# Optimization experiments

Measured on AMD Instinct MI355X. Metric: run time of the kernel, lower is better.

Reference implementation:

```python
import jax, jax.numpy as jnp
import numpy as np

N = 10000      # num nodes
E = 160000     # num edges (before self-loops)
D_IN = 512
D_HID = 512
D_OUT = 512
C = 64         # num classes


def setup_inputs() -> dict:
    key = jax.random.key(0)
    ks = jax.random.split(key, 8)
    x = jax.random.normal(ks[0], (N, D_IN), dtype=jnp.float32)
    edge_index = jax.random.randint(ks[1], (2, E), 0, N, dtype=jnp.int64)
    W1 = jax.random.normal(ks[2], (D_IN, D_HID), jnp.float32) / np.sqrt(D_IN)
    b1 = jnp.zeros((D_HID,), jnp.float32)
    W2 = jax.random.normal(ks[3], (D_HID, D_OUT), jnp.float32) / np.sqrt(D_HID)
    b2 = jnp.zeros((D_OUT,), jnp.float32)
    Wc = jax.random.normal(ks[4], (D_OUT, C), jnp.float32) / np.sqrt(D_OUT)
    bc = jnp.zeros((C,), jnp.float32)
    return {"x": x, "edge_index": edge_index, "W1": W1, "b1": b1,
            "W2": W2, "b2": b2, "Wc": Wc, "bc": bc}


def _gcn_conv(x, src, dst, ew, W, b):
    """GCNConv: symmetric degree-normalized scatter-add. ew = edge weights."""
    h = x @ W  # [N, D_out] dense GEMM
    deg = jax.ops.segment_sum(ew, dst, num_segments=N)  # in-degree incl. loops
    dis = jnp.where(deg > 0, jax.lax.rsqrt(jnp.maximum(deg, 1e-12)), 0.0)
    norm = dis[src] * dis[dst] * ew  # [E+N]
    out = jax.ops.segment_sum(h[src] * norm[:, None], dst, num_segments=N)
    return out + b


def reference(x, edge_index, W1, b1, W2, b2, Wc, bc):
    src, dst = edge_index[0], edge_index[1]
    # add_remaining_self_loops: drop existing self-loops, add one per node
    loops = jnp.arange(N, dtype=edge_index.dtype)
    src_f = jnp.concatenate([src, loops])
    dst_f = jnp.concatenate([dst, loops])
    ew = jnp.concatenate([(src != dst).astype(jnp.float32),
                          jnp.ones((N,), jnp.float32)])
    h = jax.nn.relu(_gcn_conv(x, src_f, dst_f, ew, W1, b1))
    h = _gcn_conv(h, src_f, dst_f, ew, W2, b2)
    logits = h @ Wc + bc
    return logits, jax.nn.log_softmax(logits, axis=1)
```

## Files before the change

### kernel.cpp

```cpp
#include <hip/hip_runtime.h>
#include <hip/hip_bf16.h>

#define N_NODES 10000
#define DIM 512
#define NCLS 64
#define BM 64
#define BN 128
#define BK 32
#define ELLW 64

typedef __hip_bfloat16 bf16;
typedef unsigned short u16;
typedef __attribute__((ext_vector_type(8))) short short8;
typedef __attribute__((ext_vector_type(4))) float f32x4;

__device__ __forceinline__ float b2f(bf16 v) { return __bfloat162float(v); }
__device__ __forceinline__ float ldIn(const void* p, size_t i, int isb) {
    return isb ? b2f(((const bf16*)p)[i]) : ((const float*)p)[i];
}
__device__ __forceinline__ int getE(const int* ei, int is64, int flat) {
    return is64 ? ei[2 * (size_t)flat] : ei[flat];
}
__device__ __forceinline__ void load_lds16(const bf16* g, bf16* l) {
    __builtin_amdgcn_global_load_lds(
        (const __attribute__((address_space(1))) void*)g,
        (__attribute__((address_space(3))) void*)l, 16, 0, 0);
}

__global__ void init_kernel(const u16* x16, const int* ei, int* flags, int* cursor) {
    int i = blockIdx.x * blockDim.x + threadIdx.x;
    if (i < N_NODES) cursor[i] = 0;
    if (blockIdx.x == 0 && threadIdx.x < 64) {
        int l = threadIdx.x;
        int cf = 0;
        #pragma unroll
        for (int j = 0; j < 4; j++) {
            int e = (x16[l * 4 + j] >> 7) & 0xFF;
            cf += (e >= 97 && e <= 157) ? 1 : 0;
        }
        #pragma unroll
        for (int o = 32; o > 0; o >>= 1) cf += __shfl_xor(cf, o, 64);
        int cz = (l < 32) ? ((ei[2 * l + 1] == 0) ? 1 : 0) : 0;
        #pragma unroll
        for (int o = 32; o > 0; o >>= 1) cz += __shfl_xor(cz, o, 64);
        if (l == 0) { flags[0] = (cf >= 200) ? 1 : 0; flags[1] = (cz >= 16) ? 1 : 0; }
    }
}

__global__ void fill_ell(const int* __restrict__ ei, const int* __restrict__ flags,
                         int* __restrict__ cursor, int* __restrict__ ell, int E) {
    int e = blockIdx.x * blockDim.x + threadIdx.x;
    if (e >= E) return;
    int is64 = flags[1];
    int s = getE(ei, is64, e), d = getE(ei, is64, E + e);
    if (s == d || (unsigned)s >= N_NODES || (unsigned)d >= N_NODES) return;
    int pos = atomicAdd(&cursor[d], 1);
    ell[d * ELLW + (pos & (ELLW - 1))] = s;
}

__global__ __launch_bounds__(256) void convert_all(
        const void* __restrict__ X, const void* __restrict__ W1,
        const void* __restrict__ W2, const void* __restrict__ Wc,
        const int* __restrict__ flags, const int* __restrict__ cursor,
        bf16* __restrict__ Xb, bf16* __restrict__ Wt1, bf16* __restrict__ Wt2,
        bf16* __restrict__ Wtc, float* __restrict__ dis) {
    __shared__ float tile[32][33];
    int b = blockIdx.x, t = threadIdx.x;
    int isb = flags[0];
    if (b < 2500) {
        int base = (b * 256 + t) * 8;
        bf16 o[8];
        if (isb) {
            *(uint4*)o = *(const uint4*)((const bf16*)X + base);
        } else {
            const float* Xf = (const float*)X + base;
            float4 v0 = *(const float4*)Xf, v1 = *(const float4*)(Xf + 4);
            o[0] = __float2bfloat16(v0.x); o[1] = __float2bfloat16(v0.y);
            o[2] = __float2bfloat16(v0.z); o[3] = __float2bfloat16(v0.w);
            o[4] = __float2bfloat16(v1.x); o[5] = __float2bfloat16(v1.y);
            o[6] = __float2bfloat16(v1.z); o[7] = __float2bfloat16(v1.w);
        }
        *(uint4*)&Xb[base] = *(uint4*)o;
    } else if (b < 3044) {
        const void* W; bf16* Wt; int N; int bb;
        if (b < 2756)      { W = W1; Wt = Wt1; N = DIM;  bb = b - 2500; }
        else if (b < 3012) { W = W2; Wt = Wt2; N = DIM;  bb = b - 2756; }
        else               { W = Wc; Wt = Wtc; N = NCLS; bb = b - 3012; }
        int nt = N / 32;
        int n0 = (bb % nt) * 32, k0 = (bb / nt) * 32;
        int tx = t & 31, ty = t >> 5;
        for (int r = ty; r < 32; r += 8)
            tile[r][tx] = ldIn(W, (size_t)(k0 + r) * N + n0 + tx, isb);
        __syncthreads();
        for (int r = ty; r < 32; r += 8)
            Wt[(size_t)(n0 + r) * DIM + k0 + tx] = __float2bfloat16(tile[tx][r]);
    } else {
        int base = ((b - 3044) * 256 + t) * 8;
        #pragma unroll
        for (int j = 0; j < 8; j++) {
            int n = base + j;
            if (n < N_NODES) dis[n] = rsqrtf((float)cursor[n] + 1.0f);
        }
    }
}

__global__ __launch_bounds__(256) void gemm_mfma(
        const bf16* __restrict__ A, const bf16* __restrict__ Bt,
        bf16* __restrict__ C, int M, int Nc, int K,
        const float* __restrict__ rowscale) {
    __shared__ bf16 At[BM * BK];
    __shared__ bf16 Bts[BN * BK];
    int t = threadIdx.x;
    int w = t >> 6, l = t & 63;
    int bm = blockIdx.y * BM, bn = blockIdx.x * BN;
    int wn = w * 32;

    f32x4 acc[4][2] = {};
    int srow = l >> 2;
    int sk8  = (l & 3) * 8;

    for (int k0 = 0; k0 < K; k0 += BK) {
        __syncthreads();
        load_lds16(A + (size_t)(bm + w * 16 + srow) * K + k0 + sk8, &At[w * 512]);
        #pragma unroll
        for (int half = 0; half < 2; half++) {
            int c = w + half * 4;
            load_lds16(Bt + (size_t)(bn + c * 16 + srow) * K + k0 + sk8, &Bts[c * 512]);
        }
        __syncthreads();

        short8 af[4], bf[2];
        #pragma unroll
        for (int i = 0; i < 4; i++)
            af[i] = *(const short8*)&At[(i * 16 + (l & 15)) * BK + (l >> 4) * 8];
        #pragma unroll
        for (int j = 0; j < 2; j++)
            bf[j] = *(const short8*)&Bts[(wn + j * 16 + (l & 15)) * BK + (l >> 4) * 8];
        #pragma unroll
        for (int i = 0; i < 4; i++)
            #pragma unroll
            for (int j = 0; j < 2; j++)
                acc[i][j] = __builtin_amdgcn_mfma_f32_16x16x32_bf16(
                                af[i], bf[j], acc[i][j], 0, 0, 0);
    }

    int col = l & 15, rq = (l >> 4) * 4;
    #pragma unroll
    for (int i = 0; i < 4; i++) {
        #pragma unroll
        for (int r = 0; r < 4; r++) {
            int gm = bm + i * 16 + rq + r;
            if (gm >= M) continue;
            float rs = rowscale ? rowscale[gm] : 1.0f;
            #pragma unroll
            for (int j = 0; j < 2; j++) {
                int gn = bn + wn + j * 16 + col;
                C[(size_t)gm * Nc + gn] = __float2bfloat16(acc[i][j][r] * rs);
            }
        }
    }
}

__global__ __launch_bounds__(256) void gather_ell(
        const int* __restrict__ cursor, const int* __restrict__ ell,
        const bf16* __restrict__ Hs, const float* __restrict__ dis,
        const void* __restrict__ bias, const int* __restrict__ flags,
        bf16* __restrict__ Out, int relu) {
    int wid = (int)((blockIdx.x * (size_t)blockDim.x + threadIdx.x) >> 6);
    int lane = threadIdx.x & 63;
    if (wid >= N_NODES) return;
    int cnt = min(cursor[wid], ELLW);
    int idx = ell[wid * ELLW + lane];

    float acc[8];
    bf16 v[8];
    *(uint4*)v = *(const uint4*)(Hs + (size_t)wid * DIM + lane * 8);
    #pragma unroll
    for (int j = 0; j < 8; j++) acc[j] = b2f(v[j]);

    int e = 0;
    for (; e + 7 < cnt; e += 8) {
        bf16 r[8][8];
        #pragma unroll
        for (int b = 0; b < 8; b++) {
            int s = __shfl(idx, e + b, 64);
            *(uint4*)r[b] = *(const uint4*)(Hs + (size_t)s * DIM + lane * 8);
        }
        #pragma unroll
        for (int j = 0; j < 8; j++)
            acc[j] += ((b2f(r[0][j]) + b2f(r[1][j])) + (b2f(r[2][j]) + b2f(r[3][j])))
                    + ((b2f(r[4][j]) + b2f(r[5][j])) + (b2f(r[6][j]) + b2f(r[7][j])));
    }
    for (; e < cnt; e++) {
        int s = __shfl(idx, e, 64);
        *(uint4*)v = *(const uint4*)(Hs + (size_t)s * DIM + lane * 8);
        #pragma unroll
        for (int j = 0; j < 8; j++) acc[j] += b2f(v[j]);
    }

    float ds = dis[wid];
    int ibias = flags[0];
    bf16 o[8];
    #pragma unroll
    for (int j = 0; j < 8; j++) {
        float val = acc[j] * ds + ldIn(bias, lane * 8 + j, ibias);
        if (relu) val = fmaxf(val, 0.0f);
        o[j] = __float2bfloat16(val);
    }
    *(uint4*)(Out + (size_t)wid * DIM + lane * 8) = *(uint4*)o;
}

__global__ __launch_bounds__(256) void cls_lsm_kernel(
        const bf16* __restrict__ A, const bf16* __restrict__ Wct,
        const void* __restrict__ bias, const int* __restrict__ flags,
        float* __restrict__ out, int M) {
    __shared__ bf16 Ws[NCLS * DIM];
    int t = threadIdx.x, w = t >> 6, l = t & 63;

    #pragma unroll
    for (int i = 0; i < 16; i++) {
        int c = i * 4 + w;
        load_lds16(Wct + c * 512 + l * 8, &Ws[c * 512]);
    }
    __syncthreads();

    int row0 = (blockIdx.x * 4 + w) * 16;
    int q = l >> 4, col15 = l & 15;

    f32x4 acc[4] = {};
    #pragma unroll
    for (int k0 = 0; k0 < DIM; k0 += 32) {
        short8 af = *(const short8*)&A[(size_t)(row0 + col15) * DIM + k0 + q * 8];
        #pragma unroll
        for (int j = 0; j < 4; j++) {
            short8 bf = *(const short8*)&Ws[(j * 16 + col15) * DIM + k0 + q * 8];
            acc[j] = __builtin_amdgcn_mfma_f32_16x16x32_bf16(af, bf, acc[j], 0, 0, 0);
        }
    }

    int ibias = flags[0];
    float bcol[4];
    #pragma unroll
    for (int j = 0; j < 4; j++) bcol[j] = ldIn(bias, j * 16 + col15, ibias);

    #pragma unroll
    for (int r = 0; r < 4; r++) {
        int row = row0 + q * 4 + r;
        float v[4];
        #pragma unroll
        for (int j = 0; j < 4; j++) v[j] = acc[j][r] + bcol[j];
        float m = fmaxf(fmaxf(v[0], v[1]), fmaxf(v[2], v[3]));
        #pragma unroll
        for (int o = 8; o > 0; o >>= 1) m = fmaxf(m, __shfl_xor(m, o, 64));
        float s = __expf(v[0] - m) + __expf(v[1] - m) + __expf(v[2] - m) + __expf(v[3] - m);
        #pragma unroll
        for (int o = 8; o > 0; o >>= 1) s += __shfl_xor(s, o, 64);
        float lse = m + __logf(s);
        if (row < M) {
            #pragma unroll
            for (int j = 0; j < 4; j++) {
                out[(size_t)row * NCLS + j * 16 + col15] = v[j];
                out[(size_t)M * NCLS + (size_t)row * NCLS + j * 16 + col15] = v[j] - lse;
            }
        }
    }
}

extern "C" void kernel_launch(void* const* d_in, const int* in_sizes, int n_in,
                              void* d_out, int out_size, void* d_ws, size_t ws_size,
                              hipStream_t stream) {
    const void* x  = d_in[0];
    const int*  ei = (const int*)d_in[1];
    const void* W1 = d_in[2];
    const void* b1 = d_in[3];
    const void* W2 = d_in[4];
    const void* b2 = d_in[5];
    const void* Wc = d_in[6];
    const void* bc = d_in[7];
    float* out = (float*)d_out;
    int E = in_sizes[1] / 2;

    char* ws = (char*)d_ws;
    int*   flags  = (int*)ws;
    float* dis    = (float*)(ws + 4096);
    int*   cursor = (int*)(ws + 65536);
    int*   ell    = (int*)(ws + 131072);
    bf16*  xb     = (bf16*) (ws + 4194304);
    bf16*  Wt1    = (bf16*) (ws + 14680064);
    bf16*  Wt2    = (bf16*) (ws + 15204352);
    bf16*  Wct    = (bf16*) (ws + 15728640);
    bf16*  B0     = (bf16*) (ws + 16777216);
    bf16*  B1     = (bf16*) (ws + 27262976);

    int gE = (E + 255) / 256;
    int gN = (N_NODES * 64 + 255) / 256;
    dim3 gg(DIM / BN, (N_NODES + BM - 1) / BM);

    init_kernel<<<(N_NODES + 255) / 256, 256, 0, stream>>>((const u16*)x, ei, flags, cursor);
    fill_ell<<<gE, 256, 0, stream>>>(ei, flags, cursor, ell, E);
    convert_all<<<3049, 256, 0, stream>>>(x, W1, W2, Wc, flags, cursor,
                                          xb, Wt1, Wt2, Wct, dis);

    gemm_mfma<<<gg, 256, 0, stream>>>(xb, Wt1, B0, N_NODES, DIM, DIM, dis);
    gather_ell<<<gN, 256, 0, stream>>>(cursor, ell, B0, dis, b1, flags, B1, 1);

    gemm_mfma<<<gg, 256, 0, stream>>>(B1, Wt2, B0, N_NODES, DIM, DIM, dis);
    gather_ell<<<gN, 256, 0, stream>>>(cursor, ell, B0, dis, b2, flags, B1, 0);

    cls_lsm_kernel<<<(N_NODES + 63) / 64, 256, 0, stream>>>(B1, Wct, bc, flags, out, N_NODES);
}
```

Baseline: 192.2 us.

## Fuse ELL fill into convert kernel, recompute degree scale inline, widen GEMM K tile

Moves the ELL-building edge scatter into the convert_all launch as extra blocks, which removes one kernel launch. The dis array is dropped and the normalization factor is recomputed from cursor in the GEMM epilogue and in the gather. The GEMM K tile grows from 32 to 64, halving the K-loop iterations and barriers at the cost of more LDS per block. The classifier kernel becomes one wave per 16 rows reading Wc directly from global memory instead of staging it in LDS.

```diff
diff --git a/kernel.cpp b/kernel.cpp
--- a/kernel.cpp
+++ b/kernel.cpp
@@ -6,7 +6,7 @@
 #define NCLS 64
 #define BM 64
 #define BN 128
-#define BK 32
+#define BK 64
 #define ELLW 64
 
 typedef __hip_bfloat16 bf16;
@@ -47,27 +47,17 @@
     }
 }
 
-__global__ void fill_ell(const int* __restrict__ ei, const int* __restrict__ flags,
-                         int* __restrict__ cursor, int* __restrict__ ell, int E) {
-    int e = blockIdx.x * blockDim.x + threadIdx.x;
-    if (e >= E) return;
-    int is64 = flags[1];
-    int s = getE(ei, is64, e), d = getE(ei, is64, E + e);
-    if (s == d || (unsigned)s >= N_NODES || (unsigned)d >= N_NODES) return;
-    int pos = atomicAdd(&cursor[d], 1);
-    ell[d * ELLW + (pos & (ELLW - 1))] = s;
-}
-
 __global__ __launch_bounds__(256) void convert_all(
         const void* __restrict__ X, const void* __restrict__ W1,
         const void* __restrict__ W2, const void* __restrict__ Wc,
-        const int* __restrict__ flags, const int* __restrict__ cursor,
+        const int* __restrict__ ei, const int* __restrict__ flags,
+        int* __restrict__ cursor, int* __restrict__ ell,
         bf16* __restrict__ Xb, bf16* __restrict__ Wt1, bf16* __restrict__ Wt2,
-        bf16* __restrict__ Wtc, float* __restrict__ dis) {
+        bf16* __restrict__ Wtc, int E) {
     __shared__ float tile[32][33];
     int b = blockIdx.x, t = threadIdx.x;
-    int isb = flags[0];
     if (b < 2500) {
+        int isb = flags[0];
         int base = (b * 256 + t) * 8;
         bf16 o[8];
         if (isb) {
@@ -82,6 +72,7 @@
         }
         *(uint4*)&Xb[base] = *(uint4*)o;
     } else if (b < 3044) {
+        int isb = flags[0];
         const void* W; bf16* Wt; int N; int bb;
         if (b < 2756)      { W = W1; Wt = Wt1; N = DIM;  bb = b - 2500; }
         else if (b < 3012) { W = W2; Wt = Wt2; N = DIM;  bb = b - 2756; }
@@ -95,19 +86,20 @@
         for (int r = ty; r < 32; r += 8)
             Wt[(size_t)(n0 + r) * DIM + k0 + tx] = __float2bfloat16(tile[tx][r]);
     } else {
-        int base = ((b - 3044) * 256 + t) * 8;
-        #pragma unroll
-        for (int j = 0; j < 8; j++) {
-            int n = base + j;
-            if (n < N_NODES) dis[n] = rsqrtf((float)cursor[n] + 1.0f);
-        }
+        int e = (b - 3044) * 256 + t;
+        if (e >= E) return;
+        int is64 = flags[1];
+        int s = getE(ei, is64, e), d = getE(ei, is64, E + e);
+        if (s == d || (unsigned)s >= N_NODES || (unsigned)d >= N_NODES) return;
+        int pos = atomicAdd(&cursor[d], 1);
+        ell[d * ELLW + (pos & (ELLW - 1))] = s;
     }
 }
 
 __global__ __launch_bounds__(256) void gemm_mfma(
         const bf16* __restrict__ A, const bf16* __restrict__ Bt,
         bf16* __restrict__ C, int M, int Nc, int K,
-        const float* __restrict__ rowscale) {
+        const int* __restrict__ deg) {
     __shared__ bf16 At[BM * BK];
     __shared__ bf16 Bts[BN * BK];
     int t = threadIdx.x;
@@ -116,32 +108,39 @@
     int wn = w * 32;
 
     f32x4 acc[4][2] = {};
-    int srow = l >> 2;
-    int sk8  = (l & 3) * 8;
+    int srow8 = l >> 3;
+    int sk8b  = (l & 7) * 8;
 
     for (int k0 = 0; k0 < K; k0 += BK) {
         __syncthreads();
-        load_lds16(A + (size_t)(bm + w * 16 + srow) * K + k0 + sk8, &At[w * 512]);
-        #pragma unroll
-        for (int half = 0; half < 2; half++) {
-            int c = w + half * 4;
-            load_lds16(Bt + (size_t)(bn + c * 16 + srow) * K + k0 + sk8, &Bts[c * 512]);
+        #pragma unroll
+        for (int i = 0; i < 2; i++) {
+            int c = w * 2 + i;
+            load_lds16(A + (size_t)(bm + c * 8 + srow8) * K + k0 + sk8b, &At[c * 512]);
+        }
+        #pragma unroll
+        for (int i = 0; i < 4; i++) {
+            int c = w * 4 + i;
+            load_lds16(Bt + (size_t)(bn + c * 8 + srow8) * K + k0 + sk8b, &Bts[c * 512]);
         }
         __syncthreads();
 
-        short8 af[4], bf[2];
-        #pragma unroll
-        for (int i = 0; i < 4; i++)
-            af[i] = *(const short8*)&At[(i * 16 + (l & 15)) * BK + (l >> 4) * 8];
-        #pragma unroll
-        for (int j = 0; j < 2; j++)
-            bf[j] = *(const short8*)&Bts[(wn + j * 16 + (l & 15)) * BK + (l >> 4) * 8];
-        #pragma unroll
-        for (int i = 0; i < 4; i++)
+        #pragma unroll
+        for (int kk = 0; kk < BK; kk += 32) {
+            short8 af[4], bf[2];
+            #pragma unroll
+            for (int i = 0; i < 4; i++)
+                af[i] = *(const short8*)&At[(i * 16 + (l & 15)) * BK + kk + (l >> 4) * 8];
             #pragma unroll
             for (int j = 0; j < 2; j++)
-                acc[i][j] = __builtin_amdgcn_mfma_f32_16x16x32_bf16(
-                                af[i], bf[j], acc[i][j], 0, 0, 0);
+                bf[j] = *(const short8*)&Bts[(wn + j * 16 + (l & 15)) * BK + kk + (l >> 4) * 8];
+            #pragma unroll
+            for (int i = 0; i < 4; i++)
+                #pragma unroll
+                for (int j = 0; j < 2; j++)
+                    acc[i][j] = __builtin_amdgcn_mfma_f32_16x16x32_bf16(
+                                    af[i], bf[j], acc[i][j], 0, 0, 0);
+        }
     }
 
     int col = l & 15, rq = (l >> 4) * 4;
@@ -151,7 +150,7 @@
         for (int r = 0; r < 4; r++) {
             int gm = bm + i * 16 + rq + r;
             if (gm >= M) continue;
-            float rs = rowscale ? rowscale[gm] : 1.0f;
+            float rs = rsqrtf((float)deg[gm] + 1.0f);
             #pragma unroll
             for (int j = 0; j < 2; j++) {
                 int gn = bn + wn + j * 16 + col;
@@ -163,13 +162,13 @@
 
 __global__ __launch_bounds__(256) void gather_ell(
         const int* __restrict__ cursor, const int* __restrict__ ell,
-        const bf16* __restrict__ Hs, const float* __restrict__ dis,
-        const void* __restrict__ bias, const int* __restrict__ flags,
-        bf16* __restrict__ Out, int relu) {
+        const bf16* __restrict__ Hs, const void* __restrict__ bias,
+        const int* __restrict__ flags, bf16* __restrict__ Out, int relu) {
     int wid = (int)((blockIdx.x * (size_t)blockDim.x + threadIdx.x) >> 6);
     int lane = threadIdx.x & 63;
     if (wid >= N_NODES) return;
-    int cnt = min(cursor[wid], ELLW);
+    int cnt0 = cursor[wid];
+    int cnt = min(cnt0, ELLW);
     int idx = ell[wid * ELLW + lane];
 
     float acc[8];
@@ -198,7 +197,7 @@
         for (int j = 0; j < 8; j++) acc[j] += b2f(v[j]);
     }
 
-    float ds = dis[wid];
+    float ds = rsqrtf((float)cnt0 + 1.0f);
     int ibias = flags[0];
     bf16 o[8];
     #pragma unroll
@@ -210,30 +209,21 @@
     *(uint4*)(Out + (size_t)wid * DIM + lane * 8) = *(uint4*)o;
 }
 
-__global__ __launch_bounds__(256) void cls_lsm_kernel(
+__global__ __launch_bounds__(64) void cls_lsm_kernel(
         const bf16* __restrict__ A, const bf16* __restrict__ Wct,
         const void* __restrict__ bias, const int* __restrict__ flags,
         float* __restrict__ out, int M) {
-    __shared__ bf16 Ws[NCLS * DIM];
-    int t = threadIdx.x, w = t >> 6, l = t & 63;
-
-    #pragma unroll
-    for (int i = 0; i < 16; i++) {
-        int c = i * 4 + w;
-        load_lds16(Wct + c * 512 + l * 8, &Ws[c * 512]);
-    }
-    __syncthreads();
-
-    int row0 = (blockIdx.x * 4 + w) * 16;
+    int l = threadIdx.x;
+    int row0 = blockIdx.x * 16;
     int q = l >> 4, col15 = l & 15;
 
     f32x4 acc[4] = {};
-    #pragma unroll
+    #pragma unroll 4
     for (int k0 = 0; k0 < DIM; k0 += 32) {
         short8 af = *(const short8*)&A[(size_t)(row0 + col15) * DIM + k0 + q * 8];
         #pragma unroll
         for (int j = 0; j < 4; j++) {
-            short8 bf = *(const short8*)&Ws[(j * 16 + col15) * DIM + k0 + q * 8];
+            short8 bf = *(const short8*)&Wct[(size_t)(j * 16 + col15) * DIM + k0 + q * 8];
             acc[j] = __builtin_amdgcn_mfma_f32_16x16x32_bf16(af, bf, acc[j], 0, 0, 0);
         }
     }
@@ -282,7 +272,6 @@
 
     char* ws = (char*)d_ws;
     int*   flags  = (int*)ws;
-    float* dis    = (float*)(ws + 4096);
     int*   cursor = (int*)(ws + 65536);
     int*   ell    = (int*)(ws + 131072);
     bf16*  xb     = (bf16*) (ws + 4194304);
@@ -292,20 +281,19 @@
     bf16*  B0     = (bf16*) (ws + 16777216);
     bf16*  B1     = (bf16*) (ws + 27262976);
 
-    int gE = (E + 255) / 256;
     int gN = (N_NODES * 64 + 255) / 256;
     dim3 gg(DIM / BN, (N_NODES + BM - 1) / BM);
+    int gConv = 3044 + (E + 255) / 256;
 
     init_kernel<<<(N_NODES + 255) / 256, 256, 0, stream>>>((const u16*)x, ei, flags, cursor);
-    fill_ell<<<gE, 256, 0, stream>>>(ei, flags, cursor, ell, E);
-    convert_all<<<3049, 256, 0, stream>>>(x, W1, W2, Wc, flags, cursor,
-                                          xb, Wt1, Wt2, Wct, dis);
-
-    gemm_mfma<<<gg, 256, 0, stream>>>(xb, Wt1, B0, N_NODES, DIM, DIM, dis);
-    gather_ell<<<gN, 256, 0, stream>>>(cursor, ell, B0, dis, b1, flags, B1, 1);
-
-    gemm_mfma<<<gg, 256, 0, stream>>>(B1, Wt2, B0, N_NODES, DIM, DIM, dis);
-    gather_ell<<<gN, 256, 0, stream>>>(cursor, ell, B0, dis, b2, flags, B1, 0);
-
-    cls_lsm_kernel<<<(N_NODES + 63) / 64, 256, 0, stream>>>(B1, Wct, bc, flags, out, N_NODES);
-}
+    convert_all<<<gConv, 256, 0, stream>>>(x, W1, W2, Wc, ei, flags, cursor, ell,
+                                           xb, Wt1, Wt2, Wct, E);
+
+    gemm_mfma<<<gg, 256, 0, stream>>>(xb, Wt1, B0, N_NODES, DIM, DIM, cursor);
+    gather_ell<<<gN, 256, 0, stream>>>(cursor, ell, B0, b1, flags, B1, 1);
+
+    gemm_mfma<<<gg, 256, 0, stream>>>(B1, Wt2, B0, N_NODES, DIM, DIM, cursor);
+    gather_ell<<<gN, 256, 0, stream>>>(cursor, ell, B0, b2, flags, B1, 0);
+
+    cls_lsm_kernel<<<(N_NODES + 15) / 16, 64, 0, stream>>>(B1, Wct, bc, flags, out, N_NODES);
+}
```

New measurement: 191.6 us. About the same (-0.3%).
